# Optimization experiments

Measured on AMD Instinct MI355X. Metric: run time of the kernel, lower is better.

Reference implementation:

```python
import jax, jax.numpy as jnp
import numpy as np

L, I, H = 4, 256, 512          # layers, input_size, hidden_size
SH, LH, GH = 4, 2, 2            # short/long/global heads
NH, HD, FF = SH + LH + GH, H // (SH + LH + GH), 2 * H
S, B = 1024, 8                  # seq (AST nodes), batch
EPS = 1e-5
NEG = -1e9


def _ln(x, g, b):
    m = jnp.mean(x, axis=-1, keepdims=True)
    v = jnp.var(x, axis=-1, keepdims=True)
    return (x - m) * jax.lax.rsqrt(v + EPS) * g + b


def setup_inputs() -> dict:
    key = jax.random.key(0)
    ks = jax.random.split(key, 10)
    w = lambda k, shape: jax.random.normal(k, shape, jnp.float32) * 0.02
    return {
        "nodes": jax.random.normal(ks[0], (S, B, I), jnp.float32),
        "dist": jax.random.randint(ks[1], (B, S, S), 0, 5, jnp.int32),
        "dense_w": w(ks[2], (H, I)), "dense_b": jnp.zeros((H,), jnp.float32),
        "dense_ln_g": jnp.ones((H,), jnp.float32), "dense_ln_b": jnp.zeros((H,), jnp.float32),
        "qkv_w": w(ks[3], (L, 3 * H, H)), "qkv_b": jnp.zeros((L, 3 * H), jnp.float32),
        "out_w": w(ks[4], (L, H, H)), "out_b": jnp.zeros((L, H), jnp.float32),
        "ln1_g": jnp.ones((L, H), jnp.float32), "ln1_b": jnp.zeros((L, H), jnp.float32),
        "ffn_w1": w(ks[5], (L, FF, H)), "ffn_b1": jnp.zeros((L, FF), jnp.float32),
        "ffn_w2": w(ks[6], (L, H, FF)), "ffn_b2": jnp.zeros((L, H), jnp.float32),
        "ln2_g": jnp.ones((L, H), jnp.float32), "ln2_b": jnp.zeros((L, H), jnp.float32),
        "bn_g": jnp.ones((H,), jnp.float32), "bn_b": jnp.zeros((H,), jnp.float32),
    }


def _mask_bias(dist):
    # dist: [B,S,S] int -> additive bias [B,NH,S,S]
    short = (dist == 1)[:, None]                       # [B,1,S,S]
    longm = (dist >= 1)[:, None]
    globm = jnp.broadcast_to((dist[:, 0:1, :] >= 1)[:, None], (dist.shape[0], 1, S, S))
    allowed = jnp.concatenate([
        jnp.broadcast_to(short, (dist.shape[0], SH, S, S)),
        jnp.broadcast_to(longm, (dist.shape[0], LH, S, S)),
        jnp.broadcast_to(globm, (dist.shape[0], GH, S, S)),
    ], axis=1)
    allowed = allowed | jnp.eye(S, dtype=bool)
    return jnp.where(allowed, 0.0, NEG).astype(jnp.float32)


def _forward(nodes, dist, dense_w, dense_b, dense_ln_g, dense_ln_b,
             qkv_w, qkv_b, out_w, out_b, ln1_g, ln1_b,
             ffn_w1, ffn_b1, ffn_w2, ffn_b2, ln2_g, ln2_b, bn_g, bn_b):
    x = jnp.transpose(nodes, (1, 0, 2))                # [B,S,I]
    x = _ln(x @ dense_w.T + dense_b, dense_ln_g, dense_ln_b)  # [B,S,H]
    bias = _mask_bias(dist)                            # [B,NH,S,S]
    scale = 1.0 / np.sqrt(HD)

    def layer(x, p):
        (wqkv, bqkv, wo, bo, g1, b1, w1, bf1, w2, bf2, g2, b2) = p
        qkv = x @ wqkv.T + bqkv                        # [B,S,3H]
        q, k, v = jnp.split(qkv, 3, axis=-1)
        q = q.reshape(B, S, NH, HD).transpose(0, 2, 1, 3)
        k = k.reshape(B, S, NH, HD).transpose(0, 2, 1, 3)
        v = v.reshape(B, S, NH, HD).transpose(0, 2, 1, 3)
        scores = jnp.einsum('bhqd,bhkd->bhqk', q, k) * scale + bias
        attn = jax.nn.softmax(scores, axis=-1)
        o = jnp.einsum('bhqk,bhkd->bhqd', attn, v)
        o = o.transpose(0, 2, 1, 3).reshape(B, S, H) @ wo.T + bo
        x = _ln(x + o, g1, b1)
        f = jax.nn.relu(x @ w1.T + bf1) @ w2.T + bf2
        x = _ln(x + f, g2, b2)
        return x, None

    params = (qkv_w, qkv_b, out_w, out_b, ln1_g, ln1_b,
              ffn_w1, ffn_b1, ffn_w2, ffn_b2, ln2_g, ln2_b)
    x, _ = jax.lax.scan(layer, x, params)
    hidden = x[:, 0]                                   # first token -> [B,H]
    m = jnp.mean(hidden, axis=0)
    v = jnp.var(hidden, axis=0)
    return (hidden - m) * jax.lax.rsqrt(v + EPS) * bn_g + bn_b


def reference(nodes, dist, dense_w, dense_b, dense_ln_g, dense_ln_b,
              qkv_w, qkv_b, out_w, out_b, ln1_g, ln1_b,
              ffn_w1, ffn_b1, ffn_w2, ffn_b2, ln2_g, ln2_b, bn_g, bn_b):
    return _forward(nodes, dist, dense_w, dense_b, dense_ln_g, dense_ln_b,
                    qkv_w, qkv_b, out_w, out_b, ln1_g, ln1_b,
                    ffn_w1, ffn_b1, ffn_w2, ffn_b2, ln2_g, ln2_b, bn_g, bn_b)
```

## Files before the change

kernel.cpp:

```cpp
#include <hip/hip_runtime.h>
#include <hip/hip_bf16.h>
#include <math.h>

#define LAYERS 4
#define IDIM 256
#define HDIM 512
#define NH 8
#define HD 64
#define FF 1024
#define SEQ 1024
#define BATCH 8
#define EPS 1e-5f

typedef __attribute__((ext_vector_type(8))) short short8;
typedef __attribute__((ext_vector_type(4))) short short4v;
typedef __attribute__((ext_vector_type(4))) float f32x4;
typedef __attribute__((ext_vector_type(4))) int int4v;
typedef __attribute__((ext_vector_type(4))) unsigned int uint4v;
typedef unsigned long long u64;

__device__ __forceinline__ short f2bf(float f) {
    unsigned u = __float_as_uint(f);
    u = (u + 0x7FFFu + ((u >> 16) & 1u)) >> 16;
    return (short)u;
}
__device__ __forceinline__ float bf2f(short s) {
    return __uint_as_float(((unsigned)(unsigned short)s) << 16);
}
__device__ __forceinline__ void gll16(const void* g, void* l) {
    __builtin_amdgcn_global_load_lds(
        (const __attribute__((address_space(1))) unsigned int*)g,
        (__attribute__((address_space(3))) unsigned int*)l, 16, 0, 0);
}
__device__ __forceinline__ float fexp2(float x) {
#if __has_builtin(__builtin_amdgcn_exp2f)
    return __builtin_amdgcn_exp2f(x);
#else
    return exp2f(x);
#endif
}

#define BAR() __builtin_amdgcn_s_barrier()
#define SCHED0() __builtin_amdgcn_sched_barrier(0)
#define VM4() asm volatile("s_waitcnt vmcnt(4)" ::: "memory")
#define VM2() asm volatile("s_waitcnt vmcnt(2)" ::: "memory")
#define VM0() asm volatile("s_waitcnt vmcnt(0)" ::: "memory")
#define LGKM0() asm volatile("s_waitcnt lgkmcnt(0)" ::: "memory")

#define CVT_P0 131072u
#define CVT_P1 3276800u
#define CVT_P2 4325376u
#define CVT_P3 6422528u
#define CVT_TOT 8519680u
#define PREP_W 8320
#define PREP_N 2048
__global__ __launch_bounds__(256) void prep_all(
    const float* __restrict__ s0, short* __restrict__ d0,
    const float* __restrict__ s1, short* __restrict__ d1,
    const float* __restrict__ s2, short* __restrict__ d2,
    const float* __restrict__ s3, short* __restrict__ d3,
    const float* __restrict__ s4, short* __restrict__ d4,
    const float* __restrict__ nodes, short* __restrict__ xt,
    const int* __restrict__ dist, u64* __restrict__ mS,
    u64* __restrict__ mL, u64* __restrict__ mG) {
    int blk = blockIdx.x;
    if (blk < PREP_W) {
        size_t i = ((size_t)blk * 256 + threadIdx.x) * 4;
        const float* s; short* d; size_t off;
        if (i < CVT_P0)      { s = s0; d = d0; off = i; }
        else if (i < CVT_P1) { s = s1; d = d1; off = i - CVT_P0; }
        else if (i < CVT_P2) { s = s2; d = d2; off = i - CVT_P1; }
        else if (i < CVT_P3) { s = s3; d = d3; off = i - CVT_P2; }
        else                 { s = s4; d = d4; off = i - CVT_P3; }
        f32x4 f = *(const f32x4*)(s + off);
        short4v o = {f2bf(f[0]), f2bf(f[1]), f2bf(f[2]), f2bf(f[3])};
        *(short4v*)(d + off) = o;
    } else if (blk < PREP_W + PREP_N) {
        size_t idx = ((size_t)(blk - PREP_W) * 256 + threadIdx.x) * 4;
        int i  = idx & (IDIM - 1);
        int sb = idx >> 8;
        int b  = sb & (BATCH - 1);
        int s  = sb >> 3;
        f32x4 f = *(const f32x4*)(nodes + idx);
        short4v o = {f2bf(f[0]), f2bf(f[1]), f2bf(f[2]), f2bf(f[3])};
        *(short4v*)(xt + ((size_t)b * SEQ + s) * IDIM + i) = o;
    } else {
        int blk2 = blk - (PREP_W + PREP_N);
        int b = blk2 >> 10, q = blk2 & 1023;
        int wv = threadIdx.x >> 6, lane = threadIdx.x & 63;
        const int* dp = dist + ((size_t)b * SEQ + q) * SEQ;
        size_t mbase = ((size_t)b * SEQ + q) * 16;
#pragma unroll
        for (int it = 0; it < 4; it++) {
            int w64 = it * 4 + wv;
            int d = dp[w64 * 64 + lane];
            u64 bs = __ballot(d == 1);
            u64 bl = __ballot(d >= 1);
            if (lane == 0) {
                mS[mbase + w64] = bs;
                mL[mbase + w64] = bl;
                if (q == 0) mG[b * 16 + w64] = bl;
            }
        }
    }
}

template<int BM, int BK>
__global__ __launch_bounds__(256, 2)
void gemm_bf16(const short* __restrict__ A, const short* __restrict__ W,
               const float* __restrict__ bias, short* __restrict__ C,
               short* __restrict__ vt, short* __restrict__ ktr,
               int M, int N, int K, int relu) {
    constexpr int UPR = BK / 8;
    constexpr int RPC = 512 / BK;
    __shared__ __align__(16) short As[BM * BK];
    __shared__ __align__(16) short Ws[128 * BK];
    const int tid = threadIdx.x;
    const int w = tid >> 6, lane = tid & 63;
    const int l15 = lane & 15, quad = lane >> 4;
    const int m0 = blockIdx.y * BM, n0 = blockIdx.x * 128;

    constexpr int NI = (BM == 128) ? 4 : 2;
    const int wm = (BM == 128) ? (w >> 1) * 64 : 0;
    const int wn = (BM == 128) ? (w & 1) * 64 : w * 32;

    f32x4 acc[4][NI];
#pragma unroll
    for (int mi = 0; mi < 4; mi++)
#pragma unroll
        for (int ni = 0; ni < NI; ni++) acc[mi][ni] = (f32x4){0.f, 0.f, 0.f, 0.f};

    const int r_in = (BK == 64) ? (lane >> 3) : (lane >> 4);
    const int c8   = lane & (UPR - 1);

    for (int k0 = 0; k0 < K; k0 += BK) {
#pragma unroll
        for (int rep = 0; rep < BM * BK / 2048; rep++) {
            int chunk = rep * 4 + w;
            int row = chunk * RPC + r_in;
            const short* src = A + (size_t)(m0 + row) * K + k0 + ((c8 ^ (row & (UPR - 1))) << 3);
            gll16(src, (char*)As + chunk * 1024);
        }
#pragma unroll
        for (int rep = 0; rep < 128 * BK / 2048; rep++) {
            int chunk = rep * 4 + w;
            int row = chunk * RPC + r_in;
            const short* src = W + (size_t)(n0 + row) * K + k0 + ((c8 ^ (row & (UPR - 1))) << 3);
            gll16(src, (char*)Ws + chunk * 1024);
        }
        __syncthreads();
#pragma unroll
        for (int ks = 0; ks < BK / 32; ks++) {
            short8 af[4], wf[NI];
            const int dblk = ks * 4 + quad;
#pragma unroll
            for (int mi = 0; mi < 4; mi++) {
                int row = wm + mi * 16 + l15;
                af[mi] = *(const short8*)((const char*)As + row * (BK * 2) + ((dblk ^ (row & (UPR - 1))) << 4));
            }
#pragma unroll
            for (int ni = 0; ni < NI; ni++) {
                int row = wn + ni * 16 + l15;
                wf[ni] = *(const short8*)((const char*)Ws + row * (BK * 2) + ((dblk ^ (row & (UPR - 1))) << 4));
            }
#pragma unroll
            for (int mi = 0; mi < 4; mi++)
#pragma unroll
                for (int ni = 0; ni < NI; ni++)
                    acc[mi][ni] = __builtin_amdgcn_mfma_f32_16x16x32_bf16(
                        af[mi], wf[ni], acc[mi][ni], 0, 0, 0);
        }
        __syncthreads();
    }
    if (vt && n0 >= 1024) {
#pragma unroll
        for (int ni = 0; ni < NI; ni++) {
            int n = n0 + wn + ni * 16 + l15;
            int d = n - 1024, h = d >> 6, dd = d & 63;
            float bz = bias[n];
#pragma unroll
            for (int mi = 0; mi < 4; mi++) {
                int mbase = m0 + wm + mi * 16 + quad * 4;
                int b = mbase >> 10, s = mbase & 1023;
                size_t off = ((size_t)(b * NH + h) * HD + dd) * SEQ + s;
                short4v pk;
#pragma unroll
                for (int r = 0; r < 4; r++) pk[r] = f2bf(acc[mi][ni][r] + bz);
                *(short4v*)(vt + off) = pk;
            }
        }
    } else if (ktr && n0 >= 512) {
#pragma unroll
        for (int ni = 0; ni < NI; ni++) {
            int n = n0 + wn + ni * 16 + l15;
            int d = n - 512, h = d >> 6, dd = d & 63;
            float bz = bias[n];
#pragma unroll
            for (int mi = 0; mi < 4; mi++) {
                int mbase = m0 + wm + mi * 16 + quad * 4;
                int b = mbase >> 10, s = mbase & 1023;
                size_t base = ((size_t)(b * NH + h) * SEQ + s) * HD + dd;
#pragma unroll
                for (int r = 0; r < 4; r++)
                    ktr[base + (size_t)r * HD] = f2bf(acc[mi][ni][r] + bz);
            }
        }
    } else {
#pragma unroll
        for (int ni = 0; ni < NI; ni++) {
            int n = n0 + wn + ni * 16 + l15;
            float bz = bias[n];
#pragma unroll
            for (int mi = 0; mi < 4; mi++) {
#pragma unroll
                for (int r = 0; r < 4; r++) {
                    int m = m0 + wm + mi * 16 + quad * 4 + r;
                    float v = acc[mi][ni][r] + bz;
                    if (relu) v = fmaxf(v, 0.f);
                    C[(size_t)m * N + n] = f2bf(v);
                }
            }
        }
    }
}

template<int K, bool RES>
__global__ __launch_bounds__(512, 1)
void gemm_ln(const short* __restrict__ A, const short* __restrict__ W,
             const float* __restrict__ bias, const short* __restrict__ resid,
             const float* __restrict__ g, const float* __restrict__ bta,
             short* __restrict__ Y) {
    constexpr int NCH = K / 32;
    __shared__ __align__(16) char smem[K * 64 + 98304];
    char* Apan = smem;
    char* ring = smem + K * 64;
    float* red = (float*)smem;

    const int tid = threadIdx.x, w = tid >> 6, lane = tid & 63;
    const int l15 = lane & 15, quad = lane >> 4;
    const int m0 = blockIdx.x * 32;
    const int rin8 = lane >> 3, c8 = lane & 7;
    const int swz8 = (c8 ^ rin8) << 3;

    f32x4 acc[2][4];
#pragma unroll
    for (int mi = 0; mi < 2; mi++)
#pragma unroll
        for (int j = 0; j < 4; j++) acc[mi][j] = (f32x4){0.f, 0.f, 0.f, 0.f};

    if constexpr (K == 512) {
#pragma unroll
        for (int j = 0; j < 4; j++) {
            int row = j * 8 + w;
            gll16(A + (size_t)(m0 + row) * K + ((lane ^ (row & 7)) << 3),
                  Apan + row * 1024);
        }
    } else {
#pragma unroll
        for (int j = 0; j < 2; j++) {
            int seg = j * 8 + w;
            int row = seg * 2 + (lane >> 5);
            gll16(A + (size_t)(m0 + row) * K + (((lane & 31) ^ (row & 7)) << 3),
                  Apan + seg * 1024);
        }
    }
#define GISS(c)                                                               \
    do {                                                                      \
        int rg_ = (c) & 1, kst_ = (c) >> 1;                                   \
        char* bp_ = ring + ((c) % 3) * 32768;                                 \
        _Pragma("unroll")                                                     \
        for (int j_ = 0; j_ < 4; j_++) {                                      \
            int seg_ = j_ * 8 + w;                                            \
            int ric_ = seg_ * 8 + rin8;                                       \
            gll16(W + (size_t)(rg_ * 256 + ric_) * K + kst_ * 64 + swz8,      \
                  bp_ + seg_ * 1024);                                         \
        }                                                                     \
    } while (0)

    GISS(0); GISS(1);
    VM4();
    BAR(); SCHED0();

    for (int c = 0; c < NCH; c++) {
        if (c + 2 < NCH) GISS(c + 2);
        {
            int kst = c >> 1, rg = c & 1;
            const char* bp = ring + (c % 3) * 32768;
#pragma unroll
            for (int ks = 0; ks < 2; ks++) {
                short8 af[2];
#pragma unroll
                for (int mi = 0; mi < 2; mi++) {
                    int ar = mi * 16 + l15;
                    af[mi] = *(const short8*)(Apan + ar * (K * 2) +
                        (((kst * 8 + ks * 4 + quad) ^ (ar & 7)) << 4));
                }
#pragma unroll
                for (int ni = 0; ni < 2; ni++) {
                    int rr = w * 32 + ni * 16 + l15;
                    short8 wf = *(const short8*)(bp + rr * 128 +
                        (((ks * 4 + quad) ^ (rr & 7)) << 4));
#pragma unroll
                    for (int mi = 0; mi < 2; mi++)
                        acc[mi][rg * 2 + ni] = __builtin_amdgcn_mfma_f32_16x16x32_bf16(
                            wf, af[mi], acc[mi][rg * 2 + ni], 0, 0, 0);
                }
            }
        }
        if (c + 1 < NCH) {
            if (c + 2 < NCH) VM4(); else VM0();
            BAR(); SCHED0();
        }
    }
#undef GISS
    __syncthreads();

    float sum[2] = {0.f, 0.f}, sq[2] = {0.f, 0.f};
#pragma unroll
    for (int mi = 0; mi < 2; mi++)
#pragma unroll
        for (int j = 0; j < 4; j++) {
            int nb = (j >> 1) * 256 + w * 32 + (j & 1) * 16 + quad * 4;
            f32x4 bz = *(const f32x4*)(bias + nb);
            f32x4 v;
            if (RES) {
                short4v rv = *(const short4v*)(resid + (size_t)(m0 + mi * 16 + l15) * HDIM + nb);
#pragma unroll
                for (int r = 0; r < 4; r++) v[r] = acc[mi][j][r] + bz[r] + bf2f(rv[r]);
            } else {
#pragma unroll
                for (int r = 0; r < 4; r++) v[r] = acc[mi][j][r] + bz[r];
            }
            acc[mi][j] = v;
            sum[mi] += v[0] + v[1] + v[2] + v[3];
            sq[mi]  += v[0] * v[0] + v[1] * v[1] + v[2] * v[2] + v[3] * v[3];
        }
#pragma unroll
    for (int mi = 0; mi < 2; mi++) {
        sum[mi] += __shfl_xor(sum[mi], 16); sum[mi] += __shfl_xor(sum[mi], 32);
        sq[mi]  += __shfl_xor(sq[mi], 16);  sq[mi]  += __shfl_xor(sq[mi], 32);
    }
    if (quad == 0) {
#pragma unroll
        for (int mi = 0; mi < 2; mi++) {
            red[(mi * 16 + l15) * 8 + w]       = sum[mi];
            red[256 + (mi * 16 + l15) * 8 + w] = sq[mi];
        }
    }
    __syncthreads();
    float mean[2], inv[2];
#pragma unroll
    for (int mi = 0; mi < 2; mi++) {
        f32x4 s0 = *(const f32x4*)(red + (mi * 16 + l15) * 8);
        f32x4 s1 = *(const f32x4*)(red + (mi * 16 + l15) * 8 + 4);
        f32x4 q0 = *(const f32x4*)(red + 256 + (mi * 16 + l15) * 8);
        f32x4 q1 = *(const f32x4*)(red + 256 + (mi * 16 + l15) * 8 + 4);
        float st = s0[0] + s0[1] + s0[2] + s0[3] + s1[0] + s1[1] + s1[2] + s1[3];
        float qt = q0[0] + q0[1] + q0[2] + q0[3] + q1[0] + q1[1] + q1[2] + q1[3];
        float mn = st * (1.f / HDIM);
        float vr = qt * (1.f / HDIM) - mn * mn;
        mean[mi] = mn;
        inv[mi]  = rsqrtf(vr + EPS);
    }
#pragma unroll
    for (int mi = 0; mi < 2; mi++)
#pragma unroll
        for (int j = 0; j < 4; j++) {
            int nb = (j >> 1) * 256 + w * 32 + (j & 1) * 16 + quad * 4;
            f32x4 gv = *(const f32x4*)(g + nb);
            f32x4 bv = *(const f32x4*)(bta + nb);
            short4v pk;
#pragma unroll
            for (int r = 0; r < 4; r++)
                pk[r] = f2bf((acc[mi][j][r] - mean[mi]) * inv[mi] * gv[r] + bv[r]);
            *(short4v*)(Y + (size_t)(m0 + mi * 16 + l15) * HDIM + nb) = pk;
        }
}

__global__ __launch_bounds__(512, 1)
void fused_ffn(const short* __restrict__ X, const short* __restrict__ W1,
               const float* __restrict__ b1, const short* __restrict__ W2,
               const float* __restrict__ b2, const float* __restrict__ g,
               const float* __restrict__ bta, short* __restrict__ Y) {
    __shared__ __align__(16) char smem[131072];
    char* Apan = smem;
    char* ring = smem + 32768;
    char* Hs   = smem;
    char* W2b  = smem + 65536;
    float* red = (float*)(smem + 65536);

    const int tid = threadIdx.x, w = tid >> 6, lane = tid & 63;
    const int l15 = lane & 15, quad = lane >> 4;
    const int m0 = blockIdx.x * 32;
    const int rin8 = lane >> 3, c8 = lane & 7;
    const int swz8 = (c8 ^ rin8) << 3;

    f32x4 acc1[2][8];
#pragma unroll
    for (int mi = 0; mi < 2; mi++)
#pragma unroll
        for (int j = 0; j < 8; j++) acc1[mi][j] = (f32x4){0.f, 0.f, 0.f, 0.f};

#pragma unroll
    for (int j = 0; j < 4; j++) {
        int row = j * 8 + w;
        gll16(X + (size_t)(m0 + row) * HDIM + ((lane ^ (row & 7)) << 3),
              Apan + row * 1024);
    }
#define F1ISS(c)                                                              \
    do {                                                                      \
        int rg_ = (c) & 3, kst_ = (c) >> 2;                                   \
        char* bp_ = ring + ((c) % 3) * 32768;                                 \
        _Pragma("unroll")                                                     \
        for (int j_ = 0; j_ < 4; j_++) {                                      \
            int seg_ = j_ * 8 + w;                                            \
            int ric_ = seg_ * 8 + rin8;                                       \
            gll16(W1 + (size_t)(rg_ * 256 + ric_) * HDIM + kst_ * 64 + swz8,  \
                  bp_ + seg_ * 1024);                                         \
        }                                                                     \
    } while (0)
#define F2ISS(c)                                                              \
    do {                                                                      \
        int rg_ = (c) & 1, kst_ = (c) >> 1;                                   \
        char* bp_ = W2b + ((c) & 1) * 32768;                                  \
        _Pragma("unroll")                                                     \
        for (int j_ = 0; j_ < 4; j_++) {                                      \
            int seg_ = j_ * 8 + w;                                            \
            int ric_ = seg_ * 8 + rin8;                                       \
            gll16(W2 + (size_t)(rg_ * 256 + ric_) * FF + kst_ * 64 + swz8,    \
                  bp_ + seg_ * 1024);                                         \
        }                                                                     \
    } while (0)

    F1ISS(0); F1ISS(1);
    VM4();
    BAR(); SCHED0();

    for (int c = 0; c < 32; c++) {
        if (c + 2 < 32) F1ISS(c + 2);
        {
            int kst = c >> 2, rg = c & 3;
            const char* bp = ring + (c % 3) * 32768;
#pragma unroll
            for (int ks = 0; ks < 2; ks++) {
                short8 af[2];
#pragma unroll
                for (int mi = 0; mi < 2; mi++) {
                    int ar = mi * 16 + l15;
                    af[mi] = *(const short8*)(Apan + ar * 1024 +
                        (((kst * 8 + ks * 4 + quad) ^ (ar & 7)) << 4));
                }
#pragma unroll
                for (int ni = 0; ni < 2; ni++) {
                    int rr = w * 32 + ni * 16 + l15;
                    short8 wf = *(const short8*)(bp + rr * 128 +
                        (((ks * 4 + quad) ^ (rr & 7)) << 4));
#pragma unroll
                    for (int mi = 0; mi < 2; mi++)
                        acc1[mi][rg * 2 + ni] = __builtin_amdgcn_mfma_f32_16x16x32_bf16(
                            wf, af[mi], acc1[mi][rg * 2 + ni], 0, 0, 0);
                }
            }
        }
        if (c + 1 < 32) {
            if (c + 2 < 32) VM4(); else VM0();
            BAR(); SCHED0();
        }
    }
    __syncthreads();

    F2ISS(0); F2ISS(1);
#pragma unroll
    for (int mi = 0; mi < 2; mi++)
#pragma unroll
        for (int j = 0; j < 8; j++) {
            int n = (j >> 1) * 256 + w * 32 + (j & 1) * 16 + quad * 4;
            f32x4 bz = *(const f32x4*)(b1 + n);
            short4v pk;
#pragma unroll
            for (int r = 0; r < 4; r++)
                pk[r] = f2bf(fmaxf(acc1[mi][j][r] + bz[r], 0.f));
            int row = mi * 16 + l15;
            int u = n >> 3;
            *(short4v*)(Hs + row * 2048 + ((u ^ (row & 7)) << 4) + (quad & 1) * 8) = pk;
        }
    LGKM0();
    VM4();
    BAR(); SCHED0();

    f32x4 acc2[2][4];
#pragma unroll
    for (int mi = 0; mi < 2; mi++)
#pragma unroll
        for (int j = 0; j < 4; j++) acc2[mi][j] = (f32x4){0.f, 0.f, 0.f, 0.f};

    for (int c = 0; c < 32; c++) {
        {
            int kst = c >> 1, rg = c & 1;
            const char* bp = W2b + (c & 1) * 32768;
#pragma unroll
            for (int ks = 0; ks < 2; ks++) {
                short8 af[2];
#pragma unroll
                for (int mi = 0; mi < 2; mi++) {
                    int ar = mi * 16 + l15;
                    af[mi] = *(const short8*)(Hs + ar * 2048 +
                        (((kst * 8 + ks * 4 + quad) ^ (ar & 7)) << 4));
                }
#pragma unroll
                for (int ni = 0; ni < 2; ni++) {
                    int rr = w * 32 + ni * 16 + l15;
                    short8 wf = *(const short8*)(bp + rr * 128 +
                        (((ks * 4 + quad) ^ (rr & 7)) << 4));
#pragma unroll
                    for (int mi = 0; mi < 2; mi++)
                        acc2[mi][rg * 2 + ni] = __builtin_amdgcn_mfma_f32_16x16x32_bf16(
                            wf, af[mi], acc2[mi][rg * 2 + ni], 0, 0, 0);
                }
            }
        }
        if (c + 1 < 32) {
            BAR(); SCHED0();
            if (c + 2 < 32) { F2ISS(c + 2); VM4(); } else VM0();
            BAR(); SCHED0();
        }
    }
#undef F1ISS
#undef F2ISS

    float sum[2] = {0.f, 0.f}, sq[2] = {0.f, 0.f};
#pragma unroll
    for (int mi = 0; mi < 2; mi++)
#pragma unroll
        for (int j = 0; j < 4; j++) {
            int nb = (j >> 1) * 256 + w * 32 + (j & 1) * 16 + quad * 4;
            f32x4 bz = *(const f32x4*)(b2 + nb);
            short4v rv = *(const short4v*)(X + (size_t)(m0 + mi * 16 + l15) * HDIM + nb);
            f32x4 v;
#pragma unroll
            for (int r = 0; r < 4; r++) v[r] = acc2[mi][j][r] + bz[r] + bf2f(rv[r]);
            acc2[mi][j] = v;
            sum[mi] += v[0] + v[1] + v[2] + v[3];
            sq[mi]  += v[0] * v[0] + v[1] * v[1] + v[2] * v[2] + v[3] * v[3];
        }
#pragma unroll
    for (int mi = 0; mi < 2; mi++) {
        sum[mi] += __shfl_xor(sum[mi], 16); sum[mi] += __shfl_xor(sum[mi], 32);
        sq[mi]  += __shfl_xor(sq[mi], 16);  sq[mi]  += __shfl_xor(sq[mi], 32);
    }
    if (quad == 0) {
#pragma unroll
        for (int mi = 0; mi < 2; mi++) {
            red[(mi * 16 + l15) * 8 + w]       = sum[mi];
            red[256 + (mi * 16 + l15) * 8 + w] = sq[mi];
        }
    }
    __syncthreads();
    float mean[2], inv[2];
#pragma unroll
    for (int mi = 0; mi < 2; mi++) {
        f32x4 s0 = *(const f32x4*)(red + (mi * 16 + l15) * 8);
        f32x4 s1 = *(const f32x4*)(red + (mi * 16 + l15) * 8 + 4);
        f32x4 q0 = *(const f32x4*)(red + 256 + (mi * 16 + l15) * 8);
        f32x4 q1 = *(const f32x4*)(red + 256 + (mi * 16 + l15) * 8 + 4);
        float st = s0[0] + s0[1] + s0[2] + s0[3] + s1[0] + s1[1] + s1[2] + s1[3];
        float qt = q0[0] + q0[1] + q0[2] + q0[3] + q1[0] + q1[1] + q1[2] + q1[3];
        float mn = st * (1.f / HDIM);
        float vr = qt * (1.f / HDIM) - mn * mn;
        mean[mi] = mn;
        inv[mi]  = rsqrtf(vr + EPS);
    }
#pragma unroll
    for (int mi = 0; mi < 2; mi++)
#pragma unroll
        for (int j = 0; j < 4; j++) {
            int nb = (j >> 1) * 256 + w * 32 + (j & 1) * 16 + quad * 4;
            f32x4 gv = *(const f32x4*)(g + nb);
            f32x4 bv = *(const f32x4*)(bta + nb);
            short4v pk;
#pragma unroll
            for (int r = 0; r < 4; r++)
                pk[r] = f2bf((acc2[mi][j][r] - mean[mi]) * inv[mi] * gv[r] + bv[r]);
            *(short4v*)(Y + (size_t)(m0 + mi * 16 + l15) * HDIM + nb) = pk;
        }
}

#define EXP2SC 0.18033688011112042f
__global__ __launch_bounds__(512, 4)
void attn_mfma(const short* __restrict__ qkv, const short* __restrict__ ktr,
               const short* __restrict__ vt,
               const u64* __restrict__ maskS, const u64* __restrict__ maskL,
               const u64* __restrict__ maskG, short* __restrict__ out) {
    const int tid = threadIdx.x;
    const int w = tid >> 6, lane = tid & 63, l15 = lane & 15, quad = lane >> 4;
    const int p = blockIdx.x;
    const int g_ = (p & 7) + 8 * (p >> 6);
    const int qt = ((p >> 3) & 7) * 2 + (w >> 2);
    const int b = g_ >> 3, h = g_ & 7;
    const int q = qt * 64 + (w & 3) * 16 + l15;

    __shared__ __align__(16) short Ks[128 * 64];
    __shared__ __align__(16) short Vs[128 * 64];

    short8 qf[2];
    {
        const short* qrow = qkv + ((size_t)(b * SEQ + q) * 1536) + h * 64;
#pragma unroll
        for (int ks = 0; ks < 2; ks++)
            qf[ks] = *(const short8*)(qrow + ks * 32 + quad * 8);
    }
    const u64* mrow = (h < 4) ? (maskS + ((size_t)b * SEQ + q) * 16)
                   : (h < 6) ? (maskL + ((size_t)b * SEQ + q) * 16)
                   :           (maskG + (size_t)b * 16);

    f32x4 of[4];
#pragma unroll
    for (int mt = 0; mt < 4; mt++) of[mt] = (f32x4){0.f, 0.f, 0.f, 0.f};
    float ls0 = 0.f, ls1 = 0.f;

    const int r_in = lane >> 3, c8 = lane & 7;
    const int swz = (c8 ^ r_in) << 3;
    const short* kbase = ktr + ((size_t)(b * NH + h) * SEQ) * HD + swz;
    const short* vp = vt + ((size_t)((b * NH + h) * HD) + r_in) * SEQ + swz;
    const int fsw = (l15 & 7);

    for (int kt = 0; kt < SEQ; kt += 128) {
#pragma unroll
        for (int rep = 0; rep < 2; rep++) {
            int c = rep * 8 + w;
            int pr = c * 8 + r_in;
            int pt = pr & 63;
            int key = (pr & 64) | (pt & 32) | (((pt >> 2) & 3) << 3)
                    | (((pt >> 4) & 1) << 2) | (pt & 3);
            gll16(kbase + (size_t)(kt + key) * HD, (char*)Ks + c * 1024);
        }
#pragma unroll
        for (int rep = 0; rep < 2; rep++) {
            int v = rep * 8 + w;
            gll16(vp + (size_t)((v & 7) * 8) * SEQ + kt + (v >> 3) * 64,
                  (char*)Vs + v * 1024);
        }
        VM2();
        BAR(); SCHED0();

        short8 pfrags[2][2];
#pragma unroll
        for (int t = 0; t < 2; t++) {
            f32x4 sa[4];
#pragma unroll
            for (int g = 0; g < 4; g++) sa[g] = (f32x4){0.f, 0.f, 0.f, 0.f};
#pragma unroll
            for (int ks = 0; ks < 2; ks++) {
                const int dblk = ks * 4 + quad;
#pragma unroll
                for (int g = 0; g < 4; g++) {
                    int row = t * 64 + g * 16 + l15;
                    short8 kf = *(const short8*)((const char*)Ks + row * 128 + ((dblk ^ fsw) << 4));
                    sa[g] = __builtin_amdgcn_mfma_f32_16x16x32_bf16(kf, qf[ks], sa[g], 0, 0, 0);
                }
            }
            u64 mw = mrow[(kt >> 6) + t];
            if ((q >> 6) == (kt >> 6) + t) mw |= 1ull << (q & 63);
            u64 mq2 = mw >> (quad * 8);
            unsigned mlo = (unsigned)mq2, mhi = (unsigned)(mq2 >> 32);
            float pv[4][4];
#pragma unroll
            for (int g = 0; g < 4; g++) {
                unsigned mg = ((g & 2) ? mhi : mlo) >> ((g & 1) * 4);
#pragma unroll
                for (int r = 0; r < 4; r++) {
                    float e = fexp2(sa[g][r] * EXP2SC);
                    e = ((mg >> r) & 1u) ? e : 0.f;
                    pv[g][r] = e;
                    if (g & 1) ls1 += e; else ls0 += e;
                }
            }
#pragma unroll
            for (int g32 = 0; g32 < 2; g32++) {
                uint4v pk;
                pk[0] = __builtin_amdgcn_perm(__float_as_uint(pv[2 * g32][1]),
                                              __float_as_uint(pv[2 * g32][0]), 0x07060302u);
                pk[1] = __builtin_amdgcn_perm(__float_as_uint(pv[2 * g32][3]),
                                              __float_as_uint(pv[2 * g32][2]), 0x07060302u);
                pk[2] = __builtin_amdgcn_perm(__float_as_uint(pv[2 * g32 + 1][1]),
                                              __float_as_uint(pv[2 * g32 + 1][0]), 0x07060302u);
                pk[3] = __builtin_amdgcn_perm(__float_as_uint(pv[2 * g32 + 1][3]),
                                              __float_as_uint(pv[2 * g32 + 1][2]), 0x07060302u);
                pfrags[t][g32] = __builtin_bit_cast(short8, pk);
            }
        }

        VM0();
        BAR(); SCHED0();

#pragma unroll
        for (int t = 0; t < 2; t++)
#pragma unroll
            for (int g32 = 0; g32 < 2; g32++) {
                const int u = g32 * 4 + quad;
#pragma unroll
                for (int mt = 0; mt < 4; mt++) {
                    int row = mt * 16 + l15;
                    short8 vf = *(const short8*)((const char*)Vs + t * 8192 + row * 128 + ((u ^ fsw) << 4));
                    of[mt] = __builtin_amdgcn_mfma_f32_16x16x32_bf16(vf, pfrags[t][g32], of[mt], 0, 0, 0);
                }
            }
        BAR(); SCHED0();
    }
    float lsum = ls0 + ls1;
    lsum += __shfl_xor(lsum, 16);
    lsum += __shfl_xor(lsum, 32);
    float inv = 1.f / lsum;
#pragma unroll
    for (int mt = 0; mt < 4; mt++) {
        short4v pk;
#pragma unroll
        for (int r = 0; r < 4; r++) pk[r] = f2bf(of[mt][r] * inv);
        *(short4v*)(out + ((size_t)(b * SEQ + q) * HDIM) + h * 64 + mt * 16 + quad * 4) = pk;
    }
}

__global__ __launch_bounds__(256) void final_bn(const short* __restrict__ X,
                                                const float* __restrict__ g,
                                                const float* __restrict__ bb,
                                                float* __restrict__ out) {
    int h = blockIdx.x * 256 + threadIdx.x;
    if (h >= HDIM) return;
    float vals[BATCH];
    float m = 0.f;
#pragma unroll
    for (int b = 0; b < BATCH; b++) {
        vals[b] = bf2f(X[(size_t)b * SEQ * HDIM + h]);
        m += vals[b];
    }
    m *= (1.f / BATCH);
    float v = 0.f;
#pragma unroll
    for (int b = 0; b < BATCH; b++) { float d = vals[b] - m; v += d * d; }
    v *= (1.f / BATCH);
    float inv = rsqrtf(v + EPS);
#pragma unroll
    for (int b = 0; b < BATCH; b++)
        out[b * HDIM + h] = (vals[b] - m) * inv * g[h] + bb[h];
}

extern "C" void kernel_launch(void* const* d_in, const int* in_sizes, int n_in,
                              void* d_out, int out_size, void* d_ws, size_t ws_size,
                              hipStream_t stream) {
    const float* nodes      = (const float*)d_in[0];
    const int*   dist       = (const int*)  d_in[1];
    const float* dense_w    = (const float*)d_in[2];
    const float* dense_b    = (const float*)d_in[3];
    const float* dense_ln_g = (const float*)d_in[4];
    const float* dense_ln_b = (const float*)d_in[5];
    const float* qkv_w      = (const float*)d_in[6];
    const float* qkv_b      = (const float*)d_in[7];
    const float* out_w      = (const float*)d_in[8];
    const float* out_b      = (const float*)d_in[9];
    const float* ln1_g      = (const float*)d_in[10];
    const float* ln1_b      = (const float*)d_in[11];
    const float* ffn_w1     = (const float*)d_in[12];
    const float* ffn_b1     = (const float*)d_in[13];
    const float* ffn_w2     = (const float*)d_in[14];
    const float* ffn_b2     = (const float*)d_in[15];
    const float* ln2_g      = (const float*)d_in[16];
    const float* ln2_b      = (const float*)d_in[17];
    const float* bn_g       = (const float*)d_in[18];
    const float* bn_b       = (const float*)d_in[19];
    float* out = (float*)d_out;

    const int M = BATCH * SEQ;
    const size_t MB = 1024 * 1024;
    char* ws = (char*)d_ws;
    short* Wd   = (short*)(ws + 0 * MB);
    short* Wqkv = (short*)(ws + 1 * MB);
    short* Wo   = (short*)(ws + 9 * MB);
    short* W1   = (short*)(ws + 13 * MB);
    short* W2   = (short*)(ws + 18 * MB);
    u64*   mS   = (u64*)(ws + 23 * MB);
    u64*   mL   = (u64*)(ws + 24 * MB);
    u64*   mG   = (u64*)(ws + 25 * MB);
    short* X    = (short*)(ws + 26 * MB);
    short* QKV  = (short*)(ws + 34 * MB);
    short* Vt   = (short*)(ws + 58 * MB);
    short* AT   = (short*)(ws + 66 * MB);
    short* Kt   = (short*)(ws + 74 * MB);
    short* XT   = QKV;

    prep_all<<<PREP_W + PREP_N + BATCH * SEQ, 256, 0, stream>>>(
        dense_w, Wd, qkv_w, Wqkv, out_w, Wo, ffn_w1, W1, ffn_w2, W2,
        nodes, XT, dist, mS, mL, mG);

    gemm_ln<IDIM, false><<<M / 32, 512, 0, stream>>>(
        XT, Wd, dense_b, nullptr, dense_ln_g, dense_ln_b, X);

    for (int l = 0; l < LAYERS; l++) {
        const short* wqkv = Wqkv + (size_t)l * 3 * HDIM * HDIM;
        const float* bqkv = qkv_b + (size_t)l * 3 * HDIM;
        const short* wo   = Wo + (size_t)l * HDIM * HDIM;
        const float* bo   = out_b + (size_t)l * HDIM;
        const short* w1   = W1 + (size_t)l * FF * HDIM;
        const float* b1   = ffn_b1 + (size_t)l * FF;
        const short* w2   = W2 + (size_t)l * HDIM * FF;
        const float* b2   = ffn_b2 + (size_t)l * HDIM;

        gemm_bf16<128, 128><<<dim3(3 * HDIM / 128, M / 128), 256, 0, stream>>>(
            X, wqkv, bqkv, QKV, Vt, Kt, M, 3 * HDIM, HDIM, 0);
        attn_mfma<<<512, 512, 0, stream>>>(QKV, Kt, Vt, mS, mL, mG, AT);
        gemm_ln<HDIM, true><<<M / 32, 512, 0, stream>>>(
            AT, wo, bo, X, ln1_g + l * HDIM, ln1_b + l * HDIM, X);
        fused_ffn<<<M / 32, 512, 0, stream>>>(
            X, w1, b1, w2, b2, ln2_g + l * HDIM, ln2_b + l * HDIM, X);
    }
    final_bn<<<(HDIM + 255) / 256, 256, 0, stream>>>(X, bn_g, bn_b, out);
}
```

Baseline: 560.7 us.

## Double-buffer K/V tiles in attention kernel and raise MFMA wave priority

The attention kernel now keeps two LDS buffers for K and V and issues the global-to-LDS loads for the next key tile during the current tile's work, waiting only on the older loads. The trailing barrier at the end of each iteration is removed, and s_setprio is raised around the MFMA loops. The aim is to hide global load latency behind compute. In exchange, LDS use per block doubles to 64KB and the launch-bounds occupancy hint drops from 4 to 2, so fewer blocks may fit per CU. Dropping the barrier relies on the alternating buffers to avoid races.

New measurement: 562.3 us. No clear change (+0.3%).

```diff
diff --git a/kernel.cpp b/kernel.cpp
--- a/kernel.cpp
+++ b/kernel.cpp
@@ -586,7 +586,7 @@
 }
 
 #define EXP2SC 0.18033688011112042f
-__global__ __launch_bounds__(512, 4)
+__global__ __launch_bounds__(512, 2)
 void attn_mfma(const short* __restrict__ qkv, const short* __restrict__ ktr,
                const short* __restrict__ vt,
                const u64* __restrict__ maskS, const u64* __restrict__ maskL,
@@ -599,8 +599,8 @@
     const int b = g_ >> 3, h = g_ & 7;
     const int q = qt * 64 + (w & 3) * 16 + l15;
 
-    __shared__ __align__(16) short Ks[128 * 64];
-    __shared__ __align__(16) short Vs[128 * 64];
+    __shared__ __align__(16) short Ks[2][128 * 64];
+    __shared__ __align__(16) short Vs[2][128 * 64];
 
     short8 qf[2];
     {
@@ -624,22 +624,29 @@
     const short* vp = vt + ((size_t)((b * NH + h) * HD) + r_in) * SEQ + swz;
     const int fsw = (l15 & 7);
 
+#define AISS(kt_, bf_)                                                        \
+    do {                                                                      \
+        _Pragma("unroll")                                                     \
+        for (int rep_ = 0; rep_ < 2; rep_++) {          \
+            int c_ = rep_ * 8 + w;                                            \
+            int pr_ = c_ * 8 + r_in;                                          \
+            int pt_ = pr_ & 63;                                               \
+            int key_ = (pr_ & 64) | (pt_ & 32) | (((pt_ >> 2) & 3) << 3)      \
+                     | (((pt_ >> 4) & 1) << 2) | (pt_ & 3);                   \
+            gll16(kbase + (size_t)((kt_) + key_) * HD,                        \
+                  (char*)Ks[bf_] + c_ * 1024);                                \
+        }                                                                     \
+        _Pragma("unroll")                                                     \
+        for (int rep_ = 0; rep_ < 2; rep_++) {        \
+            int v_ = rep_ * 8 + w;                                            \
+            gll16(vp + (size_t)((v_ & 7) * 8) * SEQ + (kt_) + (v_ >> 3) * 64, \
+                  (char*)Vs[bf_] + v_ * 1024);                                \
+        }                                                                     \
+    } while (0)
+
+    AISS(0, 0);
+    int cur = 0;
     for (int kt = 0; kt < SEQ; kt += 128) {
-#pragma unroll
-        for (int rep = 0; rep < 2; rep++) {
-            int c = rep * 8 + w;
-            int pr = c * 8 + r_in;
-            int pt = pr & 63;
-            int key = (pr & 64) | (pt & 32) | (((pt >> 2) & 3) << 3)
-                    | (((pt >> 4) & 1) << 2) | (pt & 3);
-            gll16(kbase + (size_t)(kt + key) * HD, (char*)Ks + c * 1024);
-        }
-#pragma unroll
-        for (int rep = 0; rep < 2; rep++) {
-            int v = rep * 8 + w;
-            gll16(vp + (size_t)((v & 7) * 8) * SEQ + kt + (v >> 3) * 64,
-                  (char*)Vs + v * 1024);
-        }
         VM2();
         BAR(); SCHED0();
 
@@ -649,16 +656,18 @@
             f32x4 sa[4];
 #pragma unroll
             for (int g = 0; g < 4; g++) sa[g] = (f32x4){0.f, 0.f, 0.f, 0.f};
+            __builtin_amdgcn_s_setprio(1);
 #pragma unroll
             for (int ks = 0; ks < 2; ks++) {
                 const int dblk = ks * 4 + quad;
 #pragma unroll
                 for (int g = 0; g < 4; g++) {
                     int row = t * 64 + g * 16 + l15;
-                    short8 kf = *(const short8*)((const char*)Ks + row * 128 + ((dblk ^ fsw) << 4));
+                    short8 kf = *(const short8*)((const char*)Ks[cur] + row * 128 + ((dblk ^ fsw) << 4));
                     sa[g] = __builtin_amdgcn_mfma_f32_16x16x32_bf16(kf, qf[ks], sa[g], 0, 0, 0);
                 }
             }
+            __builtin_amdgcn_s_setprio(0);
             u64 mw = mrow[(kt >> 6) + t];
             if ((q >> 6) == (kt >> 6) + t) mw |= 1ull << (q & 63);
             u64 mq2 = mw >> (quad * 8);
@@ -690,9 +699,11 @@
             }
         }
 
-        VM0();
+        if (kt + 128 < SEQ) { AISS(kt + 128, cur ^ 1); VM4(); }
+        else                VM0();
         BAR(); SCHED0();
 
+        __builtin_amdgcn_s_setprio(1);
 #pragma unroll
         for (int t = 0; t < 2; t++)
 #pragma unroll
@@ -701,12 +712,14 @@
 #pragma unroll
                 for (int mt = 0; mt < 4; mt++) {
                     int row = mt * 16 + l15;
-                    short8 vf = *(const short8*)((const char*)Vs + t * 8192 + row * 128 + ((u ^ fsw) << 4));
+                    short8 vf = *(const short8*)((const char*)Vs[cur] + t * 8192 + row * 128 + ((u ^ fsw) << 4));
                     of[mt] = __builtin_amdgcn_mfma_f32_16x16x32_bf16(vf, pfrags[t][g32], of[mt], 0, 0, 0);
                 }
             }
-        BAR(); SCHED0();
-    }
+        __builtin_amdgcn_s_setprio(0);
+        cur ^= 1;
+    }
+#undef AISS
     float lsum = ls0 + ls1;
     lsum += __shfl_xor(lsum, 16);
     lsum += __shfl_xor(lsum, 32);
```
